# Optimization experiments

Hardware: AMD Instinct MI355X
Metric: run time of the kernel (lower is better)

The kernel has to match this reference:

```python
import jax, jax.numpy as jnp
import numpy as np
import math

B, K, M, D = 8192, 16, 16, 256
LAMBDA_FGW = 0.5
TAU_KL = 0.1
N_OUTER = 5
N_SINKHORN = 10


def setup_inputs() -> dict:
    key = jax.random.key(0)
    ks = jax.random.split(key, 8)
    return {
        'slots_q': jax.random.normal(ks[0], (B, K, D), jnp.float32),
        'slots_r': jax.random.normal(ks[1], (B, M, D), jnp.float32),
        'mask_q': jnp.ones((B, K), jnp.float32),
        'mask_r': jnp.ones((B, M), jnp.float32),
        'centroids_q': jax.random.uniform(ks[2], (B, K, 2), jnp.float32),
        'centroids_r': jax.random.uniform(ks[3], (B, M, 2), jnp.float32),
        'W1': jax.random.normal(ks[4], (D, D), jnp.float32) * 0.05,
        'b1': jnp.zeros((D,), jnp.float32),
        'W2': jax.random.normal(ks[5], (D, D), jnp.float32) * 0.05,
        'b2': jnp.zeros((D,), jnp.float32),
        'log_eps': jnp.asarray(math.log(0.05), jnp.float32),
    }


def _pdist(a, b):
    # ||a_i - b_j||, clamped like torch: clamp(sumsq, 1e-6).sqrt()
    d2 = (jnp.sum(a * a, -1)[:, :, None] + jnp.sum(b * b, -1)[:, None, :]
          - 2.0 * jnp.einsum('bkd,bmd->bkm', a, b))
    return jnp.sqrt(jnp.clip(d2, 1e-6, None))


def reference(slots_q, slots_r, mask_q, mask_r, centroids_q, centroids_r,
              W1, b1, W2, b2, log_eps):
    proj = lambda x: jax.nn.relu(x @ W1.T + b1) @ W2.T + b2
    pq, pr = proj(slots_q), proj(slots_r)
    C = _pdist(pq, pr)                      # [B,K,M]
    Sq = _pdist(centroids_q, centroids_q)   # [B,K,K]
    Sr = _pdist(centroids_r, centroids_r)   # [B,M,M]

    mu = mask_q / (jnp.sum(mask_q, -1, keepdims=True) + 1e-8)
    nu = mask_r / (jnp.sum(mask_r, -1, keepdims=True) + 1e-8)
    T = mu[:, :, None] * nu[:, None, :]

    eps = jnp.clip(jnp.exp(log_eps), 0.01, 0.5)
    rho = TAU_KL / (TAU_KL + eps)
    log_mu = jnp.log(jnp.clip(mu, 1e-8, None))
    log_nu = jnpp = jnp.log(jnp.clip(nu, 1e-8, None))
    Sq2, Sr2 = Sq * Sq, Sr * Sr

    C_fgw = C
    for _ in range(N_OUTER):
        t1 = jnp.einsum('bkl,bl->bk', Sq2, T.sum(2))[:, :, None]
        t2 = jnp.einsum('bm,bmn->bn', T.sum(1), Sr2)[:, None, :]
        t3 = -2.0 * jnp.einsum('bkl,blm,bmn->bkn', Sq, T, Sr)
        L_gw = t1 + t2 + t3
        C_fgw = (1.0 - LAMBDA_FGW) * C + LAMBDA_FGW * L_gw
        log_K = -C_fgw / eps
        log_u = jnp.zeros_like(mu)
        log_v = jnp.zeros_like(nu)
        for _ in range(N_SINKHORN):
            log_u = rho * (log_mu - jax.nn.logsumexp(log_K + log_v[:, None, :], axis=2))
            log_v = rho * (log_nu - jax.nn.logsumexp(log_K + log_u[:, :, None], axis=1))
        T = jnp.exp(log_u[:, :, None] + log_K + log_v[:, None, :])

    cost = jnp.sum(T * C_fgw, axis=(-1, -2))
    return (jax.nn.sigmoid(-cost), T, C, cost)
```

## Files before the change

kernel.cpp:

```cpp
#include <hip/hip_runtime.h>


#define OFF_T   8192
#define OFF_C   2105344
#define OFF_CST 4202496

typedef float  f32x4  __attribute__((ext_vector_type(4)));
typedef float  f32x16 __attribute__((ext_vector_type(16)));
typedef short  s16x8  __attribute__((ext_vector_type(8)));

#define LOG2E 1.4426950408889634f

__device__ __forceinline__ float fexp2(float x) { return __builtin_amdgcn_exp2f(x); }
__device__ __forceinline__ float flog2(float x) { return __builtin_amdgcn_logf(x); }

__device__ __forceinline__ unsigned int cvt_pk_bf16(float lo, float hi) {
  unsigned int r;
  asm("v_cvt_pk_bf16_f32 %0, %1, %2" : "=v"(r) : "v"(lo), "v"(hi));
  return r;
}
__device__ __forceinline__ unsigned short cvt_bf16(float x) {
  unsigned int r;
  asm("v_cvt_pk_bf16_f32 %0, %1, %2" : "=v"(r) : "v"(x), "v"(x));
  return (unsigned short)r;
}

template <int CTRL>
__device__ __forceinline__ float dpp_add(float x) {
  return x + __int_as_float(__builtin_amdgcn_update_dpp(
      0, __float_as_int(x), CTRL, 0xf, 0xf, true));
}
template <int CTRL>
__device__ __forceinline__ float dpp_max(float x) {
  return fmaxf(x, __int_as_float(__builtin_amdgcn_update_dpp(
      0, __float_as_int(x), CTRL, 0xf, 0xf, true)));
}
__device__ __forceinline__ float row16_sum(float x) {
  x = dpp_add<0xB1>(x);  x = dpp_add<0x4E>(x);
  x = dpp_add<0x124>(x); x = dpp_add<0x128>(x);
  return x;
}
__device__ __forceinline__ float row16_max(float x) {
  x = dpp_max<0xB1>(x);  x = dpp_max<0x4E>(x);
  x = dpp_max<0x124>(x); x = dpp_max<0x128>(x);
  return x;
}
__device__ __forceinline__ float xor16_add(float x) {
  return x + __int_as_float(__builtin_amdgcn_ds_swizzle(__float_as_int(x), 0x401F));
}
__device__ __forceinline__ float xor16_max(float x) {
  return fmaxf(x, __int_as_float(__builtin_amdgcn_ds_swizzle(__float_as_int(x), 0x401F)));
}
__device__ __forceinline__ float xor32_add(float x) { return x + __shfl_xor(x, 32); }
__device__ __forceinline__ float xor32_max(float x) { return fmaxf(x, __shfl_xor(x, 32)); }

__global__ __launch_bounds__(256, 1)
void prep_w32(const float* __restrict__ W1, const float* __restrict__ W2,
              unsigned int* __restrict__ wh)
{
  const int fid  = blockIdx.x * 256 + threadIdx.x;
  const int l    = fid >> 13;
  const int s    = (fid >> 9) & 15;
  const int cg   = (fid >> 6) & 7;
  const int lane = fid & 63;
  const int col  = cg * 32 + (lane & 31);
  const int k0   = s * 16 + ((lane >> 5) << 3);
  const float* W = l ? W2 : W1;
  const float* src = W + ((size_t)col << 8) + k0;
  float4 a = *(const float4*)src;
  float4 b = *(const float4*)(src + 4);
  uint4 vh = {cvt_pk_bf16(a.x, a.y), cvt_pk_bf16(a.z, a.w),
              cvt_pk_bf16(b.x, b.y), cvt_pk_bf16(b.z, b.w)};
  ((uint4*)wh)[fid] = vh;
}

__global__ __launch_bounds__(512, 2)
void fgw_proj(const float* __restrict__ g_q,  const float* __restrict__ g_r,
              const unsigned short* __restrict__ wh,
              const float* __restrict__ g_b1, const float* __restrict__ g_b2,
              float* __restrict__ g_out)
{
  __shared__ __align__(16) float smemf[8704];
  char* sm = (char*)smemf;
  float* normL = smemf + 8192;
  const int bId0 = blockIdx.x * 2;
  const int tid  = threadIdx.x;
  const int lane = tid & 63, wid = tid >> 6;
  const int cl   = lane & 31, half = lane >> 5;

  #pragma unroll
  for (int j = 0; j < 4; ++j) {
    int idx = (j << 9) + tid;
    int bb  = idx >> 10;
    int t   = idx & 1023;
    int r   = t >> 6;
    int sg  = t & 63;
    int off = ((sg << 3) ^ ((r & 15) << 4));
    char* xb = sm + bb * 16384;
    const f32x4* xq = (const f32x4*)(g_q + (size_t)(bId0 + bb) * 4096 + (r << 8) + (sg << 2));
    const f32x4* xr = (const f32x4*)(g_r + (size_t)(bId0 + bb) * 4096 + (r << 8) + (sg << 2));
    f32x4 v0 = __builtin_nontemporal_load(xq);
    f32x4 v1 = __builtin_nontemporal_load(xr);
    {
      unsigned int* ph = (unsigned int*)(xb + r * 512 + off);
      ph[0] = cvt_pk_bf16(v0[0], v0[1]);
      ph[1] = cvt_pk_bf16(v0[2], v0[3]);
    }
    {
      unsigned int* ph = (unsigned int*)(xb + (16 + r) * 512 + off);
      ph[0] = cvt_pk_bf16(v1[0], v1[1]);
      ph[1] = cvt_pk_bf16(v1[2], v1[3]);
    }
  }
  __syncthreads();

  for (int layer = 0; layer < 2; ++layer) {
    f32x16 acc0, acc1;
    #pragma unroll
    for (int i = 0; i < 16; ++i) { acc0[i] = 0.f; acc1[i] = 0.f; }

    const float* bl_ = layer ? g_b2 : g_b1;
    const size_t base = (((size_t)layer * 16) * 8 + wid) * 64 + lane;
#define WL(KS) (*(const s16x8*)(wh + (base + (size_t)(KS) * 512) * 8))
    s16x8 w0 = WL(0), w1 = WL(1), w2 = WL(2), w3 = WL(3);
    #pragma unroll
    for (int ks = 0; ks < 16; ++ks) {
      s16x8 wn = w3;
      if (ks + 4 < 16) wn = WL(ks + 4);
      const int aoff = (((ks << 5) + (half << 4)) ^ ((cl & 15) << 4));
      s16x8 a0 = *(const s16x8*)(sm +         cl * 512 + aoff);
      s16x8 a1 = *(const s16x8*)(sm + 16384 + cl * 512 + aoff);
      acc0 = __builtin_amdgcn_mfma_f32_32x32x16_bf16(a0, w0, acc0, 0, 0, 0);
      acc1 = __builtin_amdgcn_mfma_f32_32x32x16_bf16(a1, w0, acc1, 0, 0, 0);
      w0 = w1; w1 = w2; w2 = w3; w3 = wn;
    }
#undef WL
    __syncthreads();

    const float bv  = bl_[(wid << 5) + cl];
    const int  colb = (((wid << 5) + cl) << 1);

    if (layer == 0) {
      #pragma unroll
      for (int reg = 0; reg < 16; ++reg) {
        int rr  = (reg & 3) + ((reg >> 2) << 3) + (half << 2);
        int off = colb ^ ((rr & 15) << 4);
        *(unsigned short*)(sm +         rr * 512 + off) = cvt_bf16(fmaxf(acc0[reg] + bv, 0.f));
        *(unsigned short*)(sm + 16384 + rr * 512 + off) = cvt_bf16(fmaxf(acc1[reg] + bv, 0.f));
      }
      __syncthreads();
    } else {
      #pragma unroll
      for (int reg = 0; reg < 16; ++reg) {
        int rr  = (reg & 3) + ((reg >> 2) << 3) + (half << 2);
        int off = colb ^ ((rr & 15) << 4);
        float p0 = acc0[reg] + bv, p1 = acc1[reg] + bv;
        float s0 = xor16_add(row16_sum(p0 * p0));
        float s1 = xor16_add(row16_sum(p1 * p1));
        if (cl == 0) {
          normL[(0 * 8 + wid) * 32 + rr] = s0;
          normL[(1 * 8 + wid) * 32 + rr] = s1;
        }
        *(unsigned short*)(sm +         rr * 512 + off) = cvt_bf16(p0);
        *(unsigned short*)(sm + 16384 + rr * 512 + off) = cvt_bf16(p1);
      }
      __syncthreads();
    }
  }

  const int fr = lane & 15, fg = lane >> 4;
  f32x4 accG = {0.f, 0.f, 0.f, 0.f};
  const int bbG = wid & 1, quad = wid >> 1;
  {
    char* xg = sm + bbG * 16384;
    #pragma unroll
    for (int kk = 0; kk < 2; ++kk) {
      int ks16 = (quad << 1) + kk;
      int koff = ((ks16 << 6) + (fg << 4)) ^ ((fr & 15) << 4);
      s16x8 aq = *(const s16x8*)(xg +        fr * 512 + koff);
      s16x8 br = *(const s16x8*)(xg + (16 + fr) * 512 + koff);
      accG = __builtin_amdgcn_mfma_f32_16x16x32_bf16(aq, br, accG, 0, 0, 0);
    }
  }
  __syncthreads();
  float* Gp = smemf;
  #pragma unroll
  for (int j = 0; j < 4; ++j)
    Gp[(bbG * 4 + quad) * 256 + ((fg << 2) + j) * 16 + fr] = accG[j];
  __syncthreads();

  {
    const int bbC = tid >> 8;
    const int t2  = tid & 255;
    const int tk  = t2 >> 4, tm = t2 & 15;
    float Gv = Gp[(bbC*4+0)*256 + t2] + Gp[(bbC*4+1)*256 + t2]
             + Gp[(bbC*4+2)*256 + t2] + Gp[(bbC*4+3)*256 + t2];
    float nq = 0.f, nr = 0.f;
    #pragma unroll
    for (int cc = 0; cc < 8; ++cc) {
      nq += normL[(bbC*8+cc)*32 + tk];
      nr += normL[(bbC*8+cc)*32 + 16 + tm];
    }
    float Cv = sqrtf(fmaxf(nq + nr - 2.0f * Gv, 1e-6f));
    __builtin_nontemporal_store(Cv, g_out + OFF_C + (size_t)(bId0 + bbC) * 256 + t2);
  }
}

__global__ __launch_bounds__(256, 8)
void fgw_sink(const float* __restrict__ g_mq, const float* __restrict__ g_mr,
              const float* __restrict__ g_cq, const float* __restrict__ g_cr,
              const float* __restrict__ g_leps, float* __restrict__ g_out)
{
  __shared__ __align__(16) float sk[4 * 1088];
  const int tid  = threadIdx.x, lane = tid & 63, w = tid >> 6;
  const int batch = blockIdx.x * 4 + w;
  const int m = lane & 15, g = lane >> 4;
  float* L     = sk + w * 1088;
  float* SqL   = L;        float* SrL   = L + 320;
  float* TtL   = L + 640;  float* M1L   = L + 640;
  float* lmuL  = L + 960;  float* muL   = L + 976;
  float* cqxL  = L + 992;  float* cqyL  = L + 1008;
  float* crxL  = L + 1024; float* cryL  = L + 1040;
  float* trowL = L + 1056; float* tcolL = L + 1072;

  float mqv = g_mq[(size_t)batch * 16 + m];
  float mrv = g_mr[(size_t)batch * 16 + m];
  float mu_m = mqv / (row16_sum(mqv) + 1e-8f);
  float nu_m = mrv / (row16_sum(mrv) + 1e-8f);
  float lmu_m = __logf(fmaxf(mu_m, 1e-8f));
  float lnu_m = __logf(fmaxf(nu_m, 1e-8f));
  float cqx_m = g_cq[(size_t)batch * 32 + 2 * m];
  float cqy_m = g_cq[(size_t)batch * 32 + 2 * m + 1];
  float crx_m = g_cr[(size_t)batch * 32 + 2 * m];
  float cry_m = g_cr[(size_t)batch * 32 + 2 * m + 1];
  if (g == 0) {
    lmuL[m] = lmu_m;  muL[m] = mu_m;
    cqxL[m] = cqx_m;  cqyL[m] = cqy_m;
    crxL[m] = crx_m;  cryL[m] = cry_m;
  }
  f32x4 lmu_j = *(const f32x4*)(lmuL + 4 * g);
  f32x4 mu_j  = *(const f32x4*)(muL  + 4 * g);
  f32x4 cqxj  = *(const f32x4*)(cqxL + 4 * g);
  f32x4 cqyj  = *(const f32x4*)(cqyL + 4 * g);
  f32x4 crxj  = *(const f32x4*)(crxL + 4 * g);
  f32x4 cryj  = *(const f32x4*)(cryL + 4 * g);

  float Sq2r[4], Sr2r[4];
  #pragma unroll
  for (int j = 0; j < 4; ++j) {
    float dx = cqxj[j] - cqx_m, dy = cqyj[j] - cqy_m;
    float d2 = fmaxf(dx * dx + dy * dy, 1e-6f);
    SqL[(4 * g + j) * 20 + m] = sqrtf(d2);
    Sq2r[j] = d2;
    float ex = crxj[j] - crx_m, ey = cryj[j] - cry_m;
    float e2 = fmaxf(ex * ex + ey * ey, 1e-6f);
    SrL[(4 * g + j) * 20 + m] = sqrtf(e2);
    Sr2r[j] = e2;
  }

  float C_[4];
  const float* Cp = g_out + OFF_C + (size_t)batch * 256;
  #pragma unroll
  for (int j = 0; j < 4; ++j) C_[j] = Cp[(4 * g + j) * 16 + m];
  float eps = fminf(fmaxf(__expf(g_leps[0]), 0.01f), 0.5f);
  const float inv_eps = 1.0f / eps;
  const float rho = 0.1f / (0.1f + eps);
  const float k2s = -inv_eps * LOG2E;
  float rlmu2[4];
  #pragma unroll
  for (int j = 0; j < 4; ++j) rlmu2[j] = rho * lmu_j[j] * LOG2E;
  const float rlnu2 = rho * lnu_m * LOG2E;
  float T_[4];
  #pragma unroll
  for (int j = 0; j < 4; ++j) T_[j] = mu_j[j] * nu_m;

  float Cf[4], E[4], B2[4], x2[4], v2 = 0.f;

  for (int it = 0; it < 5; ++it) {
    float trow_j[4];
    #pragma unroll
    for (int j = 0; j < 4; ++j) trow_j[j] = row16_sum(T_[j]);
    float tc = xor32_add(xor16_add(T_[0] + T_[1] + T_[2] + T_[3]));
    if (m == 0) { f32x4 tv = {trow_j[0], trow_j[1], trow_j[2], trow_j[3]};
                  *(f32x4*)(trowL + 4 * g) = tv; }
    if (g == 0) tcolL[m] = tc;
    { f32x4 tv = {T_[0], T_[1], T_[2], T_[3]};
      *(f32x4*)(TtL + m * 20 + 4 * g) = tv; }

    float trow_m = trowL[m];
    float t1_[4];
    #pragma unroll
    for (int j = 0; j < 4; ++j) t1_[j] = row16_sum(Sq2r[j] * trow_m);
    f32x4 tcv = *(const f32x4*)(tcolL + 4 * g);
    float p2 = tcv[0] * Sr2r[0] + tcv[1] * Sr2r[1] + tcv[2] * Sr2r[2] + tcv[3] * Sr2r[3];
    float t2_ = xor32_add(xor16_add(p2));

    float M1r[4] = {0.f, 0.f, 0.f, 0.f};
    #pragma unroll
    for (int l = 0; l < 16; ++l) {
      f32x4 t4 = *(const f32x4*)(TtL + l * 20 + 4 * g);
      float srv = SrL[l * 20 + m];
      M1r[0] += t4[0] * srv; M1r[1] += t4[1] * srv;
      M1r[2] += t4[2] * srv; M1r[3] += t4[3] * srv;
    }
    #pragma unroll
    for (int j = 0; j < 4; ++j) M1L[(4 * g + j) * 20 + m] = M1r[j];
    float t3_[4] = {0.f, 0.f, 0.f, 0.f};
    #pragma unroll
    for (int l = 0; l < 16; ++l) {
      f32x4 sq4 = *(const f32x4*)(SqL + l * 20 + 4 * g);
      float m1v = M1L[l * 20 + m];
      t3_[0] += sq4[0] * m1v; t3_[1] += sq4[1] * m1v;
      t3_[2] += sq4[2] * m1v; t3_[3] += sq4[3] * m1v;
    }

    #pragma unroll
    for (int j = 0; j < 4; ++j) {
      float lgw = t1_[j] + t2_ - 2.0f * t3_[j];
      Cf[j] = 0.5f * C_[j] + 0.5f * lgw;
      float lk2 = k2s * Cf[j];
      float mx2 = row16_max(lk2);
      E[j]  = fexp2(lk2 - mx2);
      B2[j] = lk2 + rlmu2[j] - rho * mx2;
    }

    v2 = 0.f;
    #pragma unroll 1
    for (int s = 0; s < 10; ++s) {
      float ev = fexp2(v2);
      #pragma unroll
      for (int j = 0; j < 4; ++j) {
        float sj = row16_sum(E[j] * ev);
        x2[j] = B2[j] - rho * flog2(sj);
      }
      float mx = fmaxf(fmaxf(x2[0], x2[1]), fmaxf(x2[2], x2[3]));
      mx = xor32_max(xor16_max(mx));
      float ss = fexp2(x2[0] - mx) + fexp2(x2[1] - mx)
               + fexp2(x2[2] - mx) + fexp2(x2[3] - mx);
      ss = xor32_add(xor16_add(ss));
      v2 = rlnu2 - rho * (mx + flog2(ss));
    }
    #pragma unroll
    for (int j = 0; j < 4; ++j) T_[j] = fexp2(x2[j] + v2);
  }

  float cp = T_[0] * Cf[0] + T_[1] * Cf[1] + T_[2] * Cf[2] + T_[3] * Cf[3];
  cp = xor32_add(xor16_add(row16_sum(cp)));
  float* To = g_out + OFF_T + (size_t)batch * 256;
  #pragma unroll
  for (int j = 0; j < 4; ++j)
    __builtin_nontemporal_store(T_[j], To + (4 * g + j) * 16 + m);
  if (lane == 0) {
    g_out[batch] = 1.0f / (1.0f + __expf(cp));
    g_out[OFF_CST + batch] = cp;
  }
}

extern "C" void kernel_launch(void* const* d_in, const int* in_sizes, int n_in,
                              void* d_out, int out_size, void* d_ws, size_t ws_size,
                              hipStream_t stream) {
  (void)in_sizes; (void)n_in; (void)out_size; (void)ws_size;
  unsigned int*   wh32 = (unsigned int*)d_ws;
  unsigned short* wh   = (unsigned short*)wh32;

  prep_w32<<<dim3(64), dim3(256), 0, stream>>>(
      (const float*)d_in[6], (const float*)d_in[8], wh32);
  fgw_proj<<<dim3(4096), dim3(512), 0, stream>>>(
      (const float*)d_in[0], (const float*)d_in[1], wh,
      (const float*)d_in[7], (const float*)d_in[9], (float*)d_out);
  fgw_sink<<<dim3(2048), dim3(256), 0, stream>>>(
      (const float*)d_in[2], (const float*)d_in[3],
      (const float*)d_in[4], (const float*)d_in[5],
      (const float*)d_in[10], (float*)d_out);
}
```

Measured before the change: 198.1 us.

## Use permlane swaps for reductions, simplify weight loads, shrink Gram epilogue to two waves

Replaces the ds_swizzle and shfl_xor cross-row reductions with the permlane16/permlane32 swap builtins where available. This keeps the reductions in VALU instead of going through LDS or bpermute. The MLP weight loads drop the manual four-deep register prefetch and load each step directly, leaving scheduling to the compiler. The Gram/C epilogue now has two waves do the full K-loop and write C directly, which removes the partial-sum shared-memory pass and two barriers. The cost is fewer waves doing that MFMA work.

Result: slower. 206.6 us (+4.3%).

```diff
diff --git a/kernel.cpp b/kernel.cpp
--- a/kernel.cpp
+++ b/kernel.cpp
@@ -8,6 +8,7 @@
 typedef float  f32x4  __attribute__((ext_vector_type(4)));
 typedef float  f32x16 __attribute__((ext_vector_type(16)));
 typedef short  s16x8  __attribute__((ext_vector_type(8)));
+typedef unsigned int u32x2 __attribute__((ext_vector_type(2)));
 
 #define LOG2E 1.4426950408889634f
 
@@ -53,6 +54,33 @@
 }
 __device__ __forceinline__ float xor32_add(float x) { return x + __shfl_xor(x, 32); }
 __device__ __forceinline__ float xor32_max(float x) { return fmaxf(x, __shfl_xor(x, 32)); }
+
+#if __has_builtin(__builtin_amdgcn_permlane16_swap)
+__device__ __forceinline__ float swap16_add(float x) {
+  u32x2 r = __builtin_amdgcn_permlane16_swap(__float_as_uint(x), __float_as_uint(x), false, false);
+  return __uint_as_float(r[0]) + __uint_as_float(r[1]);
+}
+__device__ __forceinline__ float swap16_max(float x) {
+  u32x2 r = __builtin_amdgcn_permlane16_swap(__float_as_uint(x), __float_as_uint(x), false, false);
+  return fmaxf(__uint_as_float(r[0]), __uint_as_float(r[1]));
+}
+#else
+__device__ __forceinline__ float swap16_add(float x) { return xor16_add(x); }
+__device__ __forceinline__ float swap16_max(float x) { return xor16_max(x); }
+#endif
+#if __has_builtin(__builtin_amdgcn_permlane32_swap)
+__device__ __forceinline__ float swap32_add(float x) {
+  u32x2 r = __builtin_amdgcn_permlane32_swap(__float_as_uint(x), __float_as_uint(x), false, false);
+  return __uint_as_float(r[0]) + __uint_as_float(r[1]);
+}
+__device__ __forceinline__ float swap32_max(float x) {
+  u32x2 r = __builtin_amdgcn_permlane32_swap(__float_as_uint(x), __float_as_uint(x), false, false);
+  return fmaxf(__uint_as_float(r[0]), __uint_as_float(r[1]));
+}
+#else
+__device__ __forceinline__ float swap32_add(float x) { return xor32_add(x); }
+__device__ __forceinline__ float swap32_max(float x) { return xor32_max(x); }
+#endif
 
 __global__ __launch_bounds__(256, 1)
 void prep_w32(const float* __restrict__ W1, const float* __restrict__ W2,
@@ -120,21 +148,16 @@
     for (int i = 0; i < 16; ++i) { acc0[i] = 0.f; acc1[i] = 0.f; }
 
     const float* bl_ = layer ? g_b2 : g_b1;
-    const size_t base = (((size_t)layer * 16) * 8 + wid) * 64 + lane;
-#define WL(KS) (*(const s16x8*)(wh + (base + (size_t)(KS) * 512) * 8))
-    s16x8 w0 = WL(0), w1 = WL(1), w2 = WL(2), w3 = WL(3);
     #pragma unroll
     for (int ks = 0; ks < 16; ++ks) {
-      s16x8 wn = w3;
-      if (ks + 4 < 16) wn = WL(ks + 4);
+      const size_t f0 = ((((size_t)layer * 16 + ks) * 8 + wid) * 64 + lane) * 8;
+      s16x8 bh = *(const s16x8*)(wh + f0);
       const int aoff = (((ks << 5) + (half << 4)) ^ ((cl & 15) << 4));
       s16x8 a0 = *(const s16x8*)(sm +         cl * 512 + aoff);
       s16x8 a1 = *(const s16x8*)(sm + 16384 + cl * 512 + aoff);
-      acc0 = __builtin_amdgcn_mfma_f32_32x32x16_bf16(a0, w0, acc0, 0, 0, 0);
-      acc1 = __builtin_amdgcn_mfma_f32_32x32x16_bf16(a1, w0, acc1, 0, 0, 0);
-      w0 = w1; w1 = w2; w2 = w3; w3 = wn;
-    }
-#undef WL
+      acc0 = __builtin_amdgcn_mfma_f32_32x32x16_bf16(a0, bh, acc0, 0, 0, 0);
+      acc1 = __builtin_amdgcn_mfma_f32_32x32x16_bf16(a1, bh, acc1, 0, 0, 0);
+    }
     __syncthreads();
 
     const float bv  = bl_[(wid << 5) + cl];
@@ -155,8 +178,8 @@
         int rr  = (reg & 3) + ((reg >> 2) << 3) + (half << 2);
         int off = colb ^ ((rr & 15) << 4);
         float p0 = acc0[reg] + bv, p1 = acc1[reg] + bv;
-        float s0 = xor16_add(row16_sum(p0 * p0));
-        float s1 = xor16_add(row16_sum(p1 * p1));
+        float s0 = swap16_add(row16_sum(p0 * p0));
+        float s1 = swap16_add(row16_sum(p1 * p1));
         if (cl == 0) {
           normL[(0 * 8 + wid) * 32 + rr] = s0;
           normL[(1 * 8 + wid) * 32 + rr] = s1;
@@ -168,41 +191,30 @@
     }
   }
 
-  const int fr = lane & 15, fg = lane >> 4;
-  f32x4 accG = {0.f, 0.f, 0.f, 0.f};
-  const int bbG = wid & 1, quad = wid >> 1;
+  if (wid >= 2) return;
   {
-    char* xg = sm + bbG * 16384;
-    #pragma unroll
-    for (int kk = 0; kk < 2; ++kk) {
-      int ks16 = (quad << 1) + kk;
+    const int fr = lane & 15, fg = lane >> 4;
+    char* xg = sm + wid * 16384;
+    f32x4 accG = {0.f, 0.f, 0.f, 0.f};
+    #pragma unroll
+    for (int ks16 = 0; ks16 < 8; ++ks16) {
       int koff = ((ks16 << 6) + (fg << 4)) ^ ((fr & 15) << 4);
       s16x8 aq = *(const s16x8*)(xg +        fr * 512 + koff);
       s16x8 br = *(const s16x8*)(xg + (16 + fr) * 512 + koff);
       accG = __builtin_amdgcn_mfma_f32_16x16x32_bf16(aq, br, accG, 0, 0, 0);
     }
-  }
-  __syncthreads();
-  float* Gp = smemf;
-  #pragma unroll
-  for (int j = 0; j < 4; ++j)
-    Gp[(bbG * 4 + quad) * 256 + ((fg << 2) + j) * 16 + fr] = accG[j];
-  __syncthreads();
-
-  {
-    const int bbC = tid >> 8;
-    const int t2  = tid & 255;
-    const int tk  = t2 >> 4, tm = t2 & 15;
-    float Gv = Gp[(bbC*4+0)*256 + t2] + Gp[(bbC*4+1)*256 + t2]
-             + Gp[(bbC*4+2)*256 + t2] + Gp[(bbC*4+3)*256 + t2];
-    float nq = 0.f, nr = 0.f;
-    #pragma unroll
-    for (int cc = 0; cc < 8; ++cc) {
-      nq += normL[(bbC*8+cc)*32 + tk];
-      nr += normL[(bbC*8+cc)*32 + 16 + tm];
-    }
-    float Cv = sqrtf(fmaxf(nq + nr - 2.0f * Gv, 1e-6f));
-    __builtin_nontemporal_store(Cv, g_out + OFF_C + (size_t)(bId0 + bbC) * 256 + t2);
+    float nr_ = 0.f;
+    #pragma unroll
+    for (int cg = 0; cg < 8; ++cg) nr_ += normL[(wid * 8 + cg) * 32 + 16 + fr];
+    #pragma unroll
+    for (int j = 0; j < 4; ++j) {
+      int row = (fg << 2) + j;
+      float nq_ = 0.f;
+      #pragma unroll
+      for (int cg = 0; cg < 8; ++cg) nq_ += normL[(wid * 8 + cg) * 32 + row];
+      float Cv = sqrtf(fmaxf(nq_ + nr_ - 2.0f * accG[j], 1e-6f));
+      __builtin_nontemporal_store(Cv, g_out + OFF_C + (size_t)(bId0 + wid) * 256 + row * 16 + fr);
+    }
   }
 }
 
@@ -280,7 +292,7 @@
     float trow_j[4];
     #pragma unroll
     for (int j = 0; j < 4; ++j) trow_j[j] = row16_sum(T_[j]);
-    float tc = xor32_add(xor16_add(T_[0] + T_[1] + T_[2] + T_[3]));
+    float tc = swap32_add(swap16_add(T_[0] + T_[1] + T_[2] + T_[3]));
     if (m == 0) { f32x4 tv = {trow_j[0], trow_j[1], trow_j[2], trow_j[3]};
                   *(f32x4*)(trowL + 4 * g) = tv; }
     if (g == 0) tcolL[m] = tc;
@@ -293,7 +305,7 @@
     for (int j = 0; j < 4; ++j) t1_[j] = row16_sum(Sq2r[j] * trow_m);
     f32x4 tcv = *(const f32x4*)(tcolL + 4 * g);
     float p2 = tcv[0] * Sr2r[0] + tcv[1] * Sr2r[1] + tcv[2] * Sr2r[2] + tcv[3] * Sr2r[3];
-    float t2_ = xor32_add(xor16_add(p2));
+    float t2_ = swap32_add(swap16_add(p2));
 
     float M1r[4] = {0.f, 0.f, 0.f, 0.f};
     #pragma unroll
@@ -334,10 +346,10 @@
         x2[j] = B2[j] - rho * flog2(sj);
       }
       float mx = fmaxf(fmaxf(x2[0], x2[1]), fmaxf(x2[2], x2[3]));
-      mx = xor32_max(xor16_max(mx));
+      mx = swap32_max(swap16_max(mx));
       float ss = fexp2(x2[0] - mx) + fexp2(x2[1] - mx)
                + fexp2(x2[2] - mx) + fexp2(x2[3] - mx);
-      ss = xor32_add(xor16_add(ss));
+      ss = swap32_add(swap16_add(ss));
       v2 = rlnu2 - rho * (mx + flog2(ss));
     }
     #pragma unroll
@@ -345,7 +357,7 @@
   }
 
   float cp = T_[0] * Cf[0] + T_[1] * Cf[1] + T_[2] * Cf[2] + T_[3] * Cf[3];
-  cp = xor32_add(xor16_add(row16_sum(cp)));
+  cp = swap32_add(swap16_add(row16_sum(cp)));
   float* To = g_out + OFF_T + (size_t)batch * 256;
   #pragma unroll
   for (int j = 0; j < 4; ++j)
```
